# Kernel optimization log

Measured on AMD Instinct MI355X. Metric: run time of the kernel, lower is better.

Reference implementation:

```python
import jax, jax.numpy as jnp
import numpy as np

N_NODES, N_EDGES, NODE_D, EDGE_D, EMB_D, N_GRAPHS = 50000, 800000, 128, 100, 92, 256
N_CONV, FC_D, N_FC, CUTOFF = 3, 128, 2, 6.0


def setup_inputs() -> dict:
    key = jax.random.key(0)
    ks = jax.random.split(key, 24)
    s = 0.05
    inp = {
        "z": jax.random.randint(ks[0], (N_NODES,), 0, 100, dtype=jnp.int32),
        "R": jax.random.normal(ks[1], (N_NODES, 3), dtype=jnp.float32) * 5.0,
        "edge_index": jax.random.randint(ks[2], (2, N_EDGES), 0, N_NODES, dtype=jnp.int32),
        "batch": jnp.sort(jax.random.randint(ks[3], (N_NODES,), 0, N_GRAPHS, dtype=jnp.int32)),
        # learned parameters
        "embedding": jax.random.uniform(ks[4], (100, EMB_D), dtype=jnp.float32),
        "emb_w": jax.random.normal(ks[5], (EMB_D, NODE_D), dtype=jnp.float32) * s,
        "emb_b": jnp.zeros((NODE_D,), jnp.float32),
        "conv_w": jax.random.normal(ks[6], (N_CONV, 2 * NODE_D + EDGE_D, 2 * NODE_D), dtype=jnp.float32) * s,
        "conv_b": jnp.zeros((N_CONV, 2 * NODE_D), jnp.float32),
        "ln_g": jnp.ones((N_CONV, NODE_D), jnp.float32),
        "ln_b": jnp.zeros((N_CONV, NODE_D), jnp.float32),
        "cfc_w": jax.random.normal(ks[7], (NODE_D, FC_D), dtype=jnp.float32) * s,
        "cfc_b": jnp.zeros((FC_D,), jnp.float32),
        "fc_w": jax.random.normal(ks[8], (N_FC, FC_D, FC_D), dtype=jnp.float32) * s,
        "fc_b": jnp.zeros((N_FC, FC_D), jnp.float32),
        "out_w": jax.random.normal(ks[9], (FC_D, 1), dtype=jnp.float32) * s,
        "out_b": jnp.zeros((1,), jnp.float32),
    }
    return inp


def _gaussian_smearing(d):
    offsets = jnp.linspace(0.0, CUTOFF, EDGE_D, dtype=d.dtype)  # [EDGE_D]
    coeff = -0.5 / (offsets[1] - offsets[0]) ** 2
    return jnp.exp(coeff * (d[:, None] - offsets[None, :]) ** 2)  # [E, EDGE_D]


def _layernorm(x, g, b, eps=1e-5):
    mu = x.mean(-1, keepdims=True)
    var = x.var(-1, keepdims=True)
    return (x - mu) / jnp.sqrt(var + eps) * g + b


def reference(z, R, edge_index, batch, embedding, emb_w, emb_b, conv_w, conv_b,
              ln_g, ln_b, cfc_w, cfc_b, fc_w, fc_b, out_w, out_b):
    src, dst = edge_index[0], edge_index[1]  # messages flow src(j) -> dst(i)
    d = jnp.linalg.norm(R[src] - R[dst], axis=-1)  # [E]
    edge_attr = _gaussian_smearing(d)  # [E, EDGE_D]

    x = embedding[z] @ emb_w + emb_b  # [N, NODE_D]
    n = x.shape[0]
    for l in range(conv_w.shape[0]):
        xi, xj = x[dst], x[src]  # gather [E, NODE_D]
        zc = jnp.concatenate([xi, xj, edge_attr], axis=1) @ conv_w[l] + conv_b[l]  # [E, 2*NODE_D]
        z1, z2 = jnp.split(zc, 2, axis=1)
        msg = jax.nn.sigmoid(z1) * jax.nn.softplus(z2)  # [E, NODE_D]
        agg = jax.ops.segment_sum(msg, dst, num_segments=n)  # scatter-add
        x = jax.nn.softplus(_layernorm(agg, ln_g[l], ln_b[l]) + x)

    # global mean pool over graphs
    sums = jax.ops.segment_sum(x, batch, num_segments=N_GRAPHS)
    cnts = jax.ops.segment_sum(jnp.ones((n, 1), x.dtype), batch, num_segments=N_GRAPHS)
    mol = sums / jnp.maximum(cnts, 1.0)  # [N_GRAPHS, NODE_D]

    h = jax.nn.softplus(mol @ cfc_w + cfc_b)
    for l in range(fc_w.shape[0]):
        h = jax.nn.softplus(h @ fc_w[l] + fc_b[l])
    return h @ out_w + out_b  # energy [N_GRAPHS, 1]
```

## Files before the change

### kernel.cpp

```cpp
#include <hip/hip_runtime.h>
#include <hip/hip_bf16.h>
#include <cmath>

#define N_NODES 50000
#define N_EDGES 800000
#define NODE_DIM 128
#define EDGE_DIM 100
#define EMB_DIM 92
#define N_GRAPHS 256

typedef __attribute__((ext_vector_type(8))) short short8_t;
typedef __attribute__((ext_vector_type(4))) float float4_t;

__device__ __forceinline__ float softplus_f(float v) {
    return v > 20.0f ? v : __logf(1.0f + __expf(v));
}
__device__ __forceinline__ float sigmoid_f(float v) {
    return 1.0f / (1.0f + __expf(-v));
}
__device__ __forceinline__ float bflo(unsigned u) { return __uint_as_float(u << 16); }
__device__ __forceinline__ float bfhi(unsigned u) { return __uint_as_float(u & 0xffff0000u); }
__device__ __forceinline__ float hlo(unsigned u) {
    unsigned short s = (unsigned short)(u & 0xffffu);
    _Float16 h; __builtin_memcpy(&h, &s, 2); return (float)h;
}
__device__ __forceinline__ float hhi(unsigned u) {
    unsigned short s = (unsigned short)(u >> 16);
    _Float16 h; __builtin_memcpy(&h, &s, 2); return (float)h;
}

__global__ void deg_kernel(const int* __restrict__ ei, int* __restrict__ deg) {
    int e = blockIdx.x * blockDim.x + threadIdx.x;
    if (e >= N_EDGES) return;
    atomicAdd(&deg[ei[N_EDGES + e]], 1);
}

#define SB 1024
__global__ void scan1_kernel(const int* __restrict__ deg, int* __restrict__ rp,
                             int* __restrict__ bsum) {
    __shared__ int buf[SB];
    int b = blockIdx.x, t = threadIdx.x, i = b * SB + t;
    int v = (i < N_NODES) ? deg[i] : 0;
    buf[t] = v;
    __syncthreads();
    for (int off = 1; off < SB; off <<= 1) {
        int a = (t >= off) ? buf[t - off] : 0;
        __syncthreads();
        buf[t] += a;
        __syncthreads();
    }
    if (i < N_NODES) rp[i] = buf[t] - v;
    if (t == SB - 1) bsum[b] = buf[t];
}
__global__ void scan2_kernel(int* __restrict__ bsum, int n) {
    if (threadIdx.x == 0) {
        int s = 0;
        for (int i = 0; i < n; i++) { int v = bsum[i]; bsum[i] = s; s += v; }
    }
}
__global__ void scan3_kernel(int* __restrict__ rp, const int* __restrict__ bsum) {
    int i = blockIdx.x * SB + threadIdx.x;
    if (i < N_NODES) rp[i] += bsum[blockIdx.x];
    if (i == 0) rp[N_NODES] = N_EDGES;
}

__global__ void fill_kernel(const int* __restrict__ ei, const float* __restrict__ R,
                            const int* __restrict__ row_ptr, int* __restrict__ cnt2,
                            float2* __restrict__ em) {
    int e = blockIdx.x * blockDim.x + threadIdx.x;
    if (e >= N_EDGES) return;
    int s = ei[e];
    int dst = ei[N_EDGES + e];
    float dx = R[3 * s + 0] - R[3 * dst + 0];
    float dy = R[3 * s + 1] - R[3 * dst + 1];
    float dz = R[3 * s + 2] - R[3 * dst + 2];
    float d = sqrtf(dx * dx + dy * dy + dz * dz);
    int pos = row_ptr[dst] + atomicAdd(&cnt2[dst], 1);
    em[pos] = make_float2(__int_as_float(s), d);
}

__global__ void gb_kernel(const int* __restrict__ batch, int* __restrict__ gs) {
    int i = blockIdx.x * 256 + threadIdx.x;
    if (i > N_NODES) return;
    int b = (i < N_NODES) ? batch[i] : N_GRAPHS;
    int pb = (i == 0) ? -1 : batch[i - 1];
    for (int g = pb + 1; g <= b; g++) gs[g] = i;
}

__global__ void wcvt_kernel(const float* __restrict__ conv_w, unsigned* __restrict__ Wep) {
    int i = blockIdx.x * 256 + threadIdx.x;
    if (i >= 3 * EDGE_DIM * 128) return;
    int l = i / (EDGE_DIM * 128), r = i - l * (EDGE_DIM * 128);
    int k = r >> 7, c = r & 127;
    const float* row = conv_w + (size_t)l * 356 * 256 + (size_t)(256 + k) * 256;
    __hip_bfloat16 lo = (__hip_bfloat16)row[c];
    __hip_bfloat16 hi = (__hip_bfloat16)row[128 + c];
    Wep[i] = ((unsigned)*(unsigned short*)&hi << 16) | (unsigned)*(unsigned short*)&lo;
}

__global__ void wprep_kernel(const float* __restrict__ conv_w, short* __restrict__ WbB) {
    int idx = blockIdx.x * 256 + threadIdx.x;
    if (idx >= 3 * 4 * 32 * 64 * 8) return;
    int j = idx & 7;
    int lane = (idx >> 3) & 63;
    int nt = (idx >> 9) & 31;
    int kc = (idx >> 14) & 3;
    int l = idx >> 16;
    int k = kc * 32 + (lane >> 4) * 8 + j;
    int nl = lane & 15;
    int row, col;
    if (nt < 16) { row = k; col = nt * 16 + nl; }
    else { row = 128 + k; col = (nt - 16) * 16 + nl; }
    __hip_bfloat16 bv = (__hip_bfloat16)conv_w[(size_t)l * 356 * 256 + (size_t)row * 256 + col];
    WbB[idx] = *(short*)&bv;
}

__global__ void embed_kernel(const int* __restrict__ z, const float* __restrict__ emb,
                             const float* __restrict__ emb_w, const float* __restrict__ emb_b,
                             float* __restrict__ x, __hip_bfloat16* __restrict__ xb) {
    __shared__ float er[EMB_DIM * 8];
    __shared__ int zi[8];
    int base = blockIdx.x * 8;
    int t = threadIdx.x;
    if (t < 8) zi[t] = z[base + t];
    __syncthreads();
    for (int idx = t; idx < EMB_DIM * 8; idx += 128) {
        int k = idx >> 3, j = idx & 7;
        er[idx] = emb[zi[j] * EMB_DIM + k];
    }
    __syncthreads();
    float acc[8];
    float bb = emb_b[t];
#pragma unroll
    for (int j = 0; j < 8; j++) acc[j] = bb;
    for (int k = 0; k < EMB_DIM; k++) {
        float w = emb_w[k * NODE_DIM + t];
        float4 ja = *(const float4*)&er[k * 8];
        float4 jb = *(const float4*)&er[k * 8 + 4];
        acc[0] = fmaf(w, ja.x, acc[0]); acc[1] = fmaf(w, ja.y, acc[1]);
        acc[2] = fmaf(w, ja.z, acc[2]); acc[3] = fmaf(w, ja.w, acc[3]);
        acc[4] = fmaf(w, jb.x, acc[4]); acc[5] = fmaf(w, jb.y, acc[5]);
        acc[6] = fmaf(w, jb.z, acc[6]); acc[7] = fmaf(w, jb.w, acc[7]);
    }
#pragma unroll
    for (int j = 0; j < 8; j++) {
        x[(base + j) * NODE_DIM + t] = acc[j];
        xb[(base + j) * NODE_DIM + t] = (__hip_bfloat16)acc[j];
    }
}

__global__ __launch_bounds__(256) void node_mfma_kernel(
    const __hip_bfloat16* __restrict__ xb, const short* __restrict__ WbB,
    const float* __restrict__ bl, float* __restrict__ P1f, _Float16* __restrict__ P2h) {
    int t = threadIdx.x;
    int wv = t >> 6, lane = t & 63;
    int mrow = lane & 15, q = lane >> 4;
    int base = blockIdx.x * 16;
    const short* xr = (const short*)xb + (size_t)(base + mrow) * 128 + q * 8;
    float4_t acc[8];
#pragma unroll
    for (int i = 0; i < 8; i++) acc[i] = (float4_t){0.f, 0.f, 0.f, 0.f};
#pragma unroll
    for (int kc = 0; kc < 4; kc++) {
        short8_t a = *(const short8_t*)(xr + kc * 32);
#pragma unroll
        for (int i = 0; i < 8; i++) {
            int nt = wv * 8 + i;
            short8_t b = *(const short8_t*)&WbB[((size_t)(kc * 32 + nt) * 64 + lane) * 8];
            acc[i] = __builtin_amdgcn_mfma_f32_16x16x32_bf16(a, b, acc[i], 0, 0, 0);
        }
    }
#pragma unroll
    for (int i = 0; i < 8; i++) {
        int nt = wv * 8 + i;
        int np = nt * 16 + mrow;
        if (np < 256) {
            float bb = bl[np];
            int off = 2 * (np & 127) + (np >> 7);
#pragma unroll
            for (int r = 0; r < 4; r++)
                P1f[(size_t)(base + q * 4 + r) * 256 + off] = acc[i][r] + bb;
        } else {
            int np2 = np - 256;
            int off = 2 * (np2 & 127) + (np2 >> 7);
#pragma unroll
            for (int r = 0; r < 4; r++)
                P2h[(size_t)(base + q * 4 + r) * 256 + off] = (_Float16)acc[i][r];
        }
    }
}

#define NTAP 10
__device__ __forceinline__ void edge_msg2(uint2 bu, float dv, float4 a,
                                          const uint2* __restrict__ Wc,
                                          float& acc0, float& acc1) {
    const float sp_ = 6.0f / 99.0f;
    const float inv_s = 99.0f / 6.0f;
    const float coeff = -0.5f * inv_s * inv_s;
    float z10 = a.x + hlo(bu.x), z20 = a.y + hhi(bu.x);
    float z11 = a.z + hlo(bu.y), z21 = a.w + hhi(bu.y);
    if (dv <= 6.34f) {
        int k0 = max(0, min(EDGE_DIM - NTAP, (int)ceilf(dv * inv_s - 4.5f)));
        const uint2* wr = Wc + k0 * 64;
#pragma unroll
        for (int i = 0; i < NTAP; i++) {
            float df = dv - (float)(k0 + i) * sp_;
            float ee = __expf(coeff * df * df);
            uint2 u = wr[i * 64];
            z10 = fmaf(bflo(u.x), ee, z10);
            z20 = fmaf(bfhi(u.x), ee, z20);
            z11 = fmaf(bflo(u.y), ee, z11);
            z21 = fmaf(bfhi(u.y), ee, z21);
        }
    }
    acc0 += sigmoid_f(z10) * softplus_f(z20);
    acc1 += sigmoid_f(z11) * softplus_f(z21);
}

__global__ __launch_bounds__(256) void node_edge_ln_kernel(
    const int* __restrict__ row_ptr, const float2* __restrict__ em,
    const float4* __restrict__ P1q, const uint2* __restrict__ P2q,
    const uint2* __restrict__ Weq,
    const float* __restrict__ lg, const float* __restrict__ lb,
    float* __restrict__ x, __hip_bfloat16* __restrict__ xb) {
    int node = blockIdx.x * 4 + (threadIdx.x >> 6);
    int l = threadIdx.x & 63;
    int c0 = 2 * l;
    int e0 = row_ptr[node], e1 = row_ptr[node + 1];
    float4 a = P1q[(size_t)node * 64 + l];
    const uint2* Wc = Weq + l;
    float acc0 = 0.f, acc1 = 0.f;
    uint2 bA = make_uint2(0, 0), bB = make_uint2(0, 0);
    float dvA = 0.f, dvB = 0.f;
    int srcC = 0, srcD = 0;
    float dC = 0.f, dD = 0.f;
    if (e0 < e1) {
        float2 m = em[e0];
        int s = __float_as_int(m.x); dvA = m.y;
        bA = P2q[(size_t)s * 64 + l];
    }
    if (e0 + 1 < e1) {
        float2 m = em[e0 + 1];
        int s = __float_as_int(m.x); dvB = m.y;
        bB = P2q[(size_t)s * 64 + l];
    }
    if (e0 + 2 < e1) { float2 m = em[e0 + 2]; srcC = __float_as_int(m.x); dC = m.y; }
    if (e0 + 3 < e1) { float2 m = em[e0 + 3]; srcD = __float_as_int(m.x); dD = m.y; }
    int e = e0;
    while (e < e1) {
        {
            uint2 b = bA; float dv = dvA;
            if (e + 2 < e1) { bA = P2q[(size_t)srcC * 64 + l]; dvA = dC; }
            if (e + 4 < e1) { float2 m = em[e + 4]; srcC = __float_as_int(m.x); dC = m.y; }
            edge_msg2(b, dv, a, Wc, acc0, acc1);
        }
        e++;
        if (e >= e1) break;
        {
            uint2 b = bB; float dv = dvB;
            if (e + 2 < e1) { bB = P2q[(size_t)srcD * 64 + l]; dvB = dD; }
            if (e + 4 < e1) { float2 m = em[e + 4]; srcD = __float_as_int(m.x); dD = m.y; }
            edge_msg2(b, dv, a, Wc, acc0, acc1);
        }
        e++;
    }
    float s1 = acc0 + acc1;
    float s2 = acc0 * acc0 + acc1 * acc1;
#pragma unroll
    for (int off = 32; off > 0; off >>= 1) {
        s1 += __shfl_xor(s1, off);
        s2 += __shfl_xor(s2, off);
    }
    float mu = s1 * (1.0f / 128.0f);
    float var = s2 * (1.0f / 128.0f) - mu * mu;
    float rstd = rsqrtf(fmaxf(var, 0.f) + 1e-5f);
    float2 xv = *(const float2*)&x[(size_t)node * 128 + c0];
    float2 gg = *(const float2*)&lg[c0];
    float2 bb = *(const float2*)&lb[c0];
    float r0 = softplus_f((acc0 - mu) * rstd * gg.x + bb.x + xv.x);
    float r1 = softplus_f((acc1 - mu) * rstd * gg.y + bb.y + xv.y);
    *(float2*)&x[(size_t)node * 128 + c0] = make_float2(r0, r1);
    __hip_bfloat16 h0 = (__hip_bfloat16)r0, h1 = (__hip_bfloat16)r1;
    unsigned pk = ((unsigned)*(unsigned short*)&h1 << 16) | (unsigned)*(unsigned short*)&h0;
    *(unsigned*)&xb[(size_t)node * 128 + c0] = pk;
}

__global__ void pool_head_kernel(const float* __restrict__ x, const int* __restrict__ gs,
                                 const float* __restrict__ cfc_w, const float* __restrict__ cfc_b,
                                 const float* __restrict__ fc_w, const float* __restrict__ fc_b,
                                 const float* __restrict__ out_w, const float* __restrict__ out_b,
                                 float* __restrict__ out) {
    int g = blockIdx.x, c = threadIdx.x;
    int n0 = gs[g], n1 = gs[g + 1];
    float s = 0.f;
    for (int n = n0; n < n1; n++) s += x[(size_t)n * 128 + c];
    __shared__ float h[128], h2[128];
    h[c] = s / fmaxf((float)(n1 - n0), 1.0f);
    __syncthreads();
    float acc = cfc_b[c];
    for (int k = 0; k < 128; k++) acc = fmaf(h[k], cfc_w[k * 128 + c], acc);
    h2[c] = softplus_f(acc);
    __syncthreads();
    for (int l = 0; l < 2; l++) {
        const float* W = fc_w + l * 128 * 128;
        acc = fc_b[l * 128 + c];
        for (int k = 0; k < 128; k++) acc = fmaf(h2[k], W[k * 128 + c], acc);
        __syncthreads();
        h2[c] = softplus_f(acc);
        __syncthreads();
    }
    h[c] = h2[c] * out_w[c];
    __syncthreads();
    for (int off = 64; off > 0; off >>= 1) {
        if (c < off) h[c] += h[c + off];
        __syncthreads();
    }
    if (c == 0) out[g] = h[0] + out_b[0];
}

extern "C" void kernel_launch(void* const* d_in, const int* in_sizes, int n_in,
                              void* d_out, int out_size, void* d_ws, size_t ws_size,
                              hipStream_t stream) {
    const int*   z      = (const int*)d_in[0];
    const float* R      = (const float*)d_in[1];
    const int*   ei     = (const int*)d_in[2];
    const int*   batch  = (const int*)d_in[3];
    const float* emb    = (const float*)d_in[4];
    const float* emb_w  = (const float*)d_in[5];
    const float* emb_b  = (const float*)d_in[6];
    const float* conv_w = (const float*)d_in[7];
    const float* conv_b = (const float*)d_in[8];
    const float* ln_g   = (const float*)d_in[9];
    const float* ln_b   = (const float*)d_in[10];
    const float* cfc_w  = (const float*)d_in[11];
    const float* cfc_b  = (const float*)d_in[12];
    const float* fc_w   = (const float*)d_in[13];
    const float* fc_b   = (const float*)d_in[14];
    const float* out_w  = (const float*)d_in[15];
    const float* out_b  = (const float*)d_in[16];
    float* out = (float*)d_out;

    float* ws    = (float*)d_ws;
    float* x     = ws;
    float* agg   = x + 6400000;
    float* P1f   = agg + 6400000;
    _Float16* P2h = (_Float16*)(P1f + 12800000);
    float* emf   = (float*)(P2h + 12800000);
    int* s_dst   = (int*)(emf + 1600000);
    int* row_ptr = s_dst + 800000;
    int* deg     = row_ptr + 50004;
    int* cnt2    = deg + 50000;
    int* bsum    = cnt2 + 50000;
    int* gs      = bsum + 64;
    unsigned* Wep        = (unsigned*)(gs + 260);
    short* WbB           = (short*)(Wep + 38400);
    __hip_bfloat16* xb   = (__hip_bfloat16*)(WbB + 196608);
    float2* em = (float2*)emf;

    hipMemsetAsync(deg, 0, (size_t)100000 * 4, stream);
    deg_kernel<<<(N_EDGES + 255) / 256, 256, 0, stream>>>(ei, deg);
    int nsb = (N_NODES + SB - 1) / SB;
    scan1_kernel<<<nsb, SB, 0, stream>>>(deg, row_ptr, bsum);
    scan2_kernel<<<1, 64, 0, stream>>>(bsum, nsb);
    scan3_kernel<<<nsb, SB, 0, stream>>>(row_ptr, bsum);
    fill_kernel<<<(N_EDGES + 255) / 256, 256, 0, stream>>>(ei, R, row_ptr, cnt2, em);
    gb_kernel<<<(N_NODES + 256) / 256 + 1, 256, 0, stream>>>(batch, gs);
    wcvt_kernel<<<(3 * EDGE_DIM * 128 + 255) / 256, 256, 0, stream>>>(conv_w, Wep);
    wprep_kernel<<<(3 * 4 * 32 * 64 * 8 + 255) / 256, 256, 0, stream>>>(conv_w, WbB);

    embed_kernel<<<N_NODES / 8, 128, 0, stream>>>(z, emb, emb_w, emb_b, x, xb);
    for (int l = 0; l < 3; l++) {
        node_mfma_kernel<<<N_NODES / 16, 256, 0, stream>>>(xb, WbB + (size_t)l * 65536,
                                                           conv_b + l * 256, P1f, P2h);
        node_edge_ln_kernel<<<N_NODES / 4, 256, 0, stream>>>(
            row_ptr, em, (const float4*)P1f, (const uint2*)P2h,
            (const uint2*)(Wep + (size_t)l * EDGE_DIM * 128),
            ln_g + l * 128, ln_b + l * 128, x, xb);
    }
    pool_head_kernel<<<N_GRAPHS, 128, 0, stream>>>(x, gs, cfc_w, cfc_b, fc_w, fc_b,
                                                   out_w, out_b, out);
}
```

Measured before the change: 966.1 us.

## Process four edges concurrently per wavefront with 8 channels per lane

The per-node edge-aggregation kernel is restructured so each wavefront splits into four 16-lane groups. Each group handles a different edge, and each lane covers 8 channels using 128-bit loads of P2 and the weights. Partial sums are then reduced across groups with shuffles before the layernorm. The aim is more memory-level parallelism per wave and fewer serial iterations for high-degree nodes, at the cost of higher register pressure. Padded tail edges are computed and then masked out, which wastes some work on nodes whose degree is not a multiple of four.

```diff
diff --git a/kernel.cpp b/kernel.cpp
--- a/kernel.cpp
+++ b/kernel.cpp
@@ -191,98 +191,140 @@
 }
 
 #define NTAP 10
-__device__ __forceinline__ void edge_msg2(uint2 bu, float dv, float4 a,
-                                          const uint2* __restrict__ Wc,
-                                          float& acc0, float& acc1) {
+__global__ __launch_bounds__(256) void node_edge_ln_kernel(
+    const int* __restrict__ row_ptr, const float2* __restrict__ em,
+    const float4* __restrict__ P1v, const uint4* __restrict__ P2v,
+    const uint4* __restrict__ Wev,
+    const float* __restrict__ lg, const float* __restrict__ lb,
+    float* __restrict__ x, __hip_bfloat16* __restrict__ xb) {
     const float sp_ = 6.0f / 99.0f;
     const float inv_s = 99.0f / 6.0f;
     const float coeff = -0.5f * inv_s * inv_s;
-    float z10 = a.x + hlo(bu.x), z20 = a.y + hhi(bu.x);
-    float z11 = a.z + hlo(bu.y), z21 = a.w + hhi(bu.y);
-    if (dv <= 6.34f) {
-        int k0 = max(0, min(EDGE_DIM - NTAP, (int)ceilf(dv * inv_s - 4.5f)));
-        const uint2* wr = Wc + k0 * 64;
-#pragma unroll
-        for (int i = 0; i < NTAP; i++) {
-            float df = dv - (float)(k0 + i) * sp_;
-            float ee = __expf(coeff * df * df);
-            uint2 u = wr[i * 64];
-            z10 = fmaf(bflo(u.x), ee, z10);
-            z20 = fmaf(bfhi(u.x), ee, z20);
-            z11 = fmaf(bflo(u.y), ee, z11);
-            z21 = fmaf(bfhi(u.y), ee, z21);
-        }
-    }
-    acc0 += sigmoid_f(z10) * softplus_f(z20);
-    acc1 += sigmoid_f(z11) * softplus_f(z21);
-}
-
-__global__ __launch_bounds__(256) void node_edge_ln_kernel(
-    const int* __restrict__ row_ptr, const float2* __restrict__ em,
-    const float4* __restrict__ P1q, const uint2* __restrict__ P2q,
-    const uint2* __restrict__ Weq,
-    const float* __restrict__ lg, const float* __restrict__ lb,
-    float* __restrict__ x, __hip_bfloat16* __restrict__ xb) {
     int node = blockIdx.x * 4 + (threadIdx.x >> 6);
     int l = threadIdx.x & 63;
-    int c0 = 2 * l;
+    int g = l >> 4, i = l & 15;
     int e0 = row_ptr[node], e1 = row_ptr[node + 1];
-    float4 a = P1q[(size_t)node * 64 + l];
-    const uint2* Wc = Weq + l;
-    float acc0 = 0.f, acc1 = 0.f;
-    uint2 bA = make_uint2(0, 0), bB = make_uint2(0, 0);
-    float dvA = 0.f, dvB = 0.f;
-    int srcC = 0, srcD = 0;
-    float dC = 0.f, dD = 0.f;
+    float4 A0 = P1v[(size_t)node * 64 + 2 * i];
+    float4 A1 = P1v[(size_t)node * 64 + 2 * i + 1];
+    float4 A2 = P1v[(size_t)node * 64 + 32 + 2 * i];
+    float4 A3 = P1v[(size_t)node * 64 + 33 + 2 * i];
+    float4 accP = make_float4(0.f, 0.f, 0.f, 0.f);
+    float4 accQ = make_float4(0.f, 0.f, 0.f, 0.f);
+
     if (e0 < e1) {
-        float2 m = em[e0];
-        int s = __float_as_int(m.x); dvA = m.y;
-        bA = P2q[(size_t)s * 64 + l];
-    }
-    if (e0 + 1 < e1) {
-        float2 m = em[e0 + 1];
-        int s = __float_as_int(m.x); dvB = m.y;
-        bB = P2q[(size_t)s * 64 + l];
-    }
-    if (e0 + 2 < e1) { float2 m = em[e0 + 2]; srcC = __float_as_int(m.x); dC = m.y; }
-    if (e0 + 3 < e1) { float2 m = em[e0 + 3]; srcD = __float_as_int(m.x); dD = m.y; }
-    int e = e0;
-    while (e < e1) {
-        {
-            uint2 b = bA; float dv = dvA;
-            if (e + 2 < e1) { bA = P2q[(size_t)srcC * 64 + l]; dvA = dC; }
-            if (e + 4 < e1) { float2 m = em[e + 4]; srcC = __float_as_int(m.x); dC = m.y; }
-            edge_msg2(b, dv, a, Wc, acc0, acc1);
+        int emax = e1 - 1;
+        int srcA, srcB; float dvAm, dvBm;
+        uint4 dA0, dA1, dB0, dB1; float dvAd, dvBd;
+        { float2 m = em[min(e0 + g, emax)];      srcA = __float_as_int(m.x); dvAm = m.y; }
+        { float2 m = em[min(e0 + 4 + g, emax)];  srcB = __float_as_int(m.x); dvBm = m.y; }
+        dA0 = P2v[(size_t)srcA * 32 + i]; dA1 = P2v[(size_t)srcA * 32 + 16 + i]; dvAd = dvAm;
+        { float2 m = em[min(e0 + 8 + g, emax)];  srcA = __float_as_int(m.x); dvAm = m.y; }
+        dB0 = P2v[(size_t)srcB * 32 + i]; dB1 = P2v[(size_t)srcB * 32 + 16 + i]; dvBd = dvBm;
+        { float2 m = em[min(e0 + 12 + g, emax)]; srcB = __float_as_int(m.x); dvBm = m.y; }
+
+#define PHASE(S, eb_)                                                             \
+        {                                                                         \
+            uint4 d0 = d##S##0, d1 = d##S##1; float dvv = dv##S##d;               \
+            d##S##0 = P2v[(size_t)src##S * 32 + i];                               \
+            d##S##1 = P2v[(size_t)src##S * 32 + 16 + i];                          \
+            dv##S##d = dv##S##m;                                                  \
+            { float2 m = em[min((eb_) + 16 + g, emax)];                           \
+              src##S = __float_as_int(m.x); dv##S##m = m.y; }                     \
+            float vm = ((eb_) + g < e1) ? 1.0f : 0.0f;                            \
+            float z10 = A0.x + hlo(d0.x), z20 = A0.y + hhi(d0.x);                 \
+            float z11 = A0.z + hlo(d0.y), z21 = A0.w + hhi(d0.y);                 \
+            float z12 = A1.x + hlo(d0.z), z22 = A1.y + hhi(d0.z);                 \
+            float z13 = A1.z + hlo(d0.w), z23 = A1.w + hhi(d0.w);                 \
+            float z14 = A2.x + hlo(d1.x), z24 = A2.y + hhi(d1.x);                 \
+            float z15 = A2.z + hlo(d1.y), z25 = A2.w + hhi(d1.y);                 \
+            float z16 = A3.x + hlo(d1.z), z26 = A3.y + hhi(d1.z);                 \
+            float z17 = A3.z + hlo(d1.w), z27 = A3.w + hhi(d1.w);                 \
+            if (dvv <= 6.34f) {                                                   \
+                int k0 = max(0, min(EDGE_DIM - NTAP, (int)ceilf(dvv * inv_s - 4.5f))); \
+                const uint4* wr = Wev + k0 * 32 + i;                              \
+                _Pragma("unroll")                                                 \
+                for (int t_ = 0; t_ < NTAP; t_++) {                               \
+                    uint4 w0 = wr[t_ * 32]; uint4 w1 = wr[t_ * 32 + 16];          \
+                    float df = dvv - (float)(k0 + t_) * sp_;                      \
+                    float ee = __expf(coeff * df * df);                           \
+                    z10 = fmaf(bflo(w0.x), ee, z10); z20 = fmaf(bfhi(w0.x), ee, z20); \
+                    z11 = fmaf(bflo(w0.y), ee, z11); z21 = fmaf(bfhi(w0.y), ee, z21); \
+                    z12 = fmaf(bflo(w0.z), ee, z12); z22 = fmaf(bfhi(w0.z), ee, z22); \
+                    z13 = fmaf(bflo(w0.w), ee, z13); z23 = fmaf(bfhi(w0.w), ee, z23); \
+                    z14 = fmaf(bflo(w1.x), ee, z14); z24 = fmaf(bfhi(w1.x), ee, z24); \
+                    z15 = fmaf(bflo(w1.y), ee, z15); z25 = fmaf(bfhi(w1.y), ee, z25); \
+                    z16 = fmaf(bflo(w1.z), ee, z16); z26 = fmaf(bfhi(w1.z), ee, z26); \
+                    z17 = fmaf(bflo(w1.w), ee, z17); z27 = fmaf(bfhi(w1.w), ee, z27); \
+                }                                                                 \
+            }                                                                     \
+            accP.x += vm * sigmoid_f(z10) * softplus_f(z20);                      \
+            accP.y += vm * sigmoid_f(z11) * softplus_f(z21);                      \
+            accP.z += vm * sigmoid_f(z12) * softplus_f(z22);                      \
+            accP.w += vm * sigmoid_f(z13) * softplus_f(z23);                      \
+            accQ.x += vm * sigmoid_f(z14) * softplus_f(z24);                      \
+            accQ.y += vm * sigmoid_f(z15) * softplus_f(z25);                      \
+            accQ.z += vm * sigmoid_f(z16) * softplus_f(z26);                      \
+            accQ.w += vm * sigmoid_f(z17) * softplus_f(z27);                      \
         }
-        e++;
-        if (e >= e1) break;
-        {
-            uint2 b = bB; float dv = dvB;
-            if (e + 2 < e1) { bB = P2q[(size_t)srcD * 64 + l]; dvB = dD; }
-            if (e + 4 < e1) { float2 m = em[e + 4]; srcD = __float_as_int(m.x); dD = m.y; }
-            edge_msg2(b, dv, a, Wc, acc0, acc1);
+
+        int eb = e0;
+        while (true) {
+            PHASE(A, eb);
+            eb += 4; if (eb >= e1) break;
+            PHASE(B, eb);
+            eb += 4; if (eb >= e1) break;
         }
-        e++;
-    }
-    float s1 = acc0 + acc1;
-    float s2 = acc0 * acc0 + acc1 * acc1;
-#pragma unroll
-    for (int off = 32; off > 0; off >>= 1) {
+#undef PHASE
+    }
+
+    accP.x += __shfl_xor(accP.x, 16); accP.x += __shfl_xor(accP.x, 32);
+    accP.y += __shfl_xor(accP.y, 16); accP.y += __shfl_xor(accP.y, 32);
+    accP.z += __shfl_xor(accP.z, 16); accP.z += __shfl_xor(accP.z, 32);
+    accP.w += __shfl_xor(accP.w, 16); accP.w += __shfl_xor(accP.w, 32);
+    accQ.x += __shfl_xor(accQ.x, 16); accQ.x += __shfl_xor(accQ.x, 32);
+    accQ.y += __shfl_xor(accQ.y, 16); accQ.y += __shfl_xor(accQ.y, 32);
+    accQ.z += __shfl_xor(accQ.z, 16); accQ.z += __shfl_xor(accQ.z, 32);
+    accQ.w += __shfl_xor(accQ.w, 16); accQ.w += __shfl_xor(accQ.w, 32);
+    float s1 = accP.x + accP.y + accP.z + accP.w + accQ.x + accQ.y + accQ.z + accQ.w;
+    float s2 = accP.x * accP.x + accP.y * accP.y + accP.z * accP.z + accP.w * accP.w +
+               accQ.x * accQ.x + accQ.y * accQ.y + accQ.z * accQ.z + accQ.w * accQ.w;
+#pragma unroll
+    for (int off = 8; off > 0; off >>= 1) {
         s1 += __shfl_xor(s1, off);
         s2 += __shfl_xor(s2, off);
     }
     float mu = s1 * (1.0f / 128.0f);
     float var = s2 * (1.0f / 128.0f) - mu * mu;
     float rstd = rsqrtf(fmaxf(var, 0.f) + 1e-5f);
-    float2 xv = *(const float2*)&x[(size_t)node * 128 + c0];
-    float2 gg = *(const float2*)&lg[c0];
-    float2 bb = *(const float2*)&lb[c0];
-    float r0 = softplus_f((acc0 - mu) * rstd * gg.x + bb.x + xv.x);
-    float r1 = softplus_f((acc1 - mu) * rstd * gg.y + bb.y + xv.y);
-    *(float2*)&x[(size_t)node * 128 + c0] = make_float2(r0, r1);
-    __hip_bfloat16 h0 = (__hip_bfloat16)r0, h1 = (__hip_bfloat16)r1;
-    unsigned pk = ((unsigned)*(unsigned short*)&h1 << 16) | (unsigned)*(unsigned short*)&h0;
-    *(unsigned*)&xb[(size_t)node * 128 + c0] = pk;
+    float4 xv1 = *(const float4*)&x[(size_t)node * 128 + 4 * i];
+    float4 xv2 = *(const float4*)&x[(size_t)node * 128 + 64 + 4 * i];
+    float4 g1 = *(const float4*)&lg[4 * i];
+    float4 g2 = *(const float4*)&lg[64 + 4 * i];
+    float4 b1 = *(const float4*)&lb[4 * i];
+    float4 b2 = *(const float4*)&lb[64 + 4 * i];
+    float r0 = softplus_f((accP.x - mu) * rstd * g1.x + b1.x + xv1.x);
+    float r1 = softplus_f((accP.y - mu) * rstd * g1.y + b1.y + xv1.y);
+    float r2 = softplus_f((accP.z - mu) * rstd * g1.z + b1.z + xv1.z);
+    float r3 = softplus_f((accP.w - mu) * rstd * g1.w + b1.w + xv1.w);
+    float r4 = softplus_f((accQ.x - mu) * rstd * g2.x + b2.x + xv2.x);
+    float r5 = softplus_f((accQ.y - mu) * rstd * g2.y + b2.y + xv2.y);
+    float r6 = softplus_f((accQ.z - mu) * rstd * g2.z + b2.z + xv2.z);
+    float r7 = softplus_f((accQ.w - mu) * rstd * g2.w + b2.w + xv2.w);
+    if (g == 0) {
+        *(float4*)&x[(size_t)node * 128 + 4 * i] = make_float4(r0, r1, r2, r3);
+        *(float4*)&x[(size_t)node * 128 + 64 + 4 * i] = make_float4(r4, r5, r6, r7);
+        __hip_bfloat16 h0 = (__hip_bfloat16)r0, h1 = (__hip_bfloat16)r1;
+        __hip_bfloat16 h2 = (__hip_bfloat16)r2, h3 = (__hip_bfloat16)r3;
+        __hip_bfloat16 h4 = (__hip_bfloat16)r4, h5 = (__hip_bfloat16)r5;
+        __hip_bfloat16 h6 = (__hip_bfloat16)r6, h7 = (__hip_bfloat16)r7;
+        uint2 pk1, pk2;
+        pk1.x = ((unsigned)*(unsigned short*)&h1 << 16) | (unsigned)*(unsigned short*)&h0;
+        pk1.y = ((unsigned)*(unsigned short*)&h3 << 16) | (unsigned)*(unsigned short*)&h2;
+        pk2.x = ((unsigned)*(unsigned short*)&h5 << 16) | (unsigned)*(unsigned short*)&h4;
+        pk2.y = ((unsigned)*(unsigned short*)&h7 << 16) | (unsigned)*(unsigned short*)&h6;
+        *(uint2*)&xb[(size_t)node * 128 + 4 * i] = pk1;
+        *(uint2*)&xb[(size_t)node * 128 + 64 + 4 * i] = pk2;
+    }
 }
 
 __global__ void pool_head_kernel(const float* __restrict__ x, const int* __restrict__ gs,
@@ -373,8 +415,8 @@
         node_mfma_kernel<<<N_NODES / 16, 256, 0, stream>>>(xb, WbB + (size_t)l * 65536,
                                                            conv_b + l * 256, P1f, P2h);
         node_edge_ln_kernel<<<N_NODES / 4, 256, 0, stream>>>(
-            row_ptr, em, (const float4*)P1f, (const uint2*)P2h,
-            (const uint2*)(Wep + (size_t)l * EDGE_DIM * 128),
+            row_ptr, em, (const float4*)P1f, (const uint4*)P2h,
+            (const uint4*)(Wep + (size_t)l * EDGE_DIM * 128),
             ln_g + l * 128, ln_b + l * 128, x, xb);
     }
     pool_head_kernel<<<N_GRAPHS, 128, 0, stream>>>(x, gs, cfc_w, cfc_b, fc_w, fc_b,
```

Result: slower. 1.009 ms (+4.4%).

## Stage edge weights in LDS and deepen gather prefetch pipeline in edge kernel

Applied to the files above, without the earlier changes.

The edge-aggregation kernel now copies the per-layer bf16 edge weight slice (about 51 KB) into shared memory and reads the taps from LDS instead of global memory. The per-edge metadata and source-row gathers are software-pipelined in batches of 8 edges with two ping-pong register sets and scheduling barriers. Edge indices and row bounds are scalarized with readfirstlane so the gather addresses use scalar registers. The large LDS footprint and register count may lower occupancy, and each 4-node block repeats the weight copy.

```diff
diff --git a/kernel.cpp b/kernel.cpp
--- a/kernel.cpp
+++ b/kernel.cpp
@@ -191,79 +191,129 @@
 }
 
 #define NTAP 10
-__device__ __forceinline__ void edge_msg2(uint2 bu, float dv, float4 a,
-                                          const uint2* __restrict__ Wc,
-                                          float& acc0, float& acc1) {
+__global__ __launch_bounds__(256) void node_edge_ln_kernel(
+    const int* __restrict__ row_ptr, const float2* __restrict__ em,
+    const float4* __restrict__ P1v, const uint2* __restrict__ P2q,
+    const unsigned* __restrict__ Wep,
+    const float* __restrict__ lg, const float* __restrict__ lb,
+    float* __restrict__ x, __hip_bfloat16* __restrict__ xb) {
+    __shared__ unsigned WeL[EDGE_DIM * 128];
+    {
+        const uint4* s4 = (const uint4*)Wep;
+        uint4* d4 = (uint4*)WeL;
+        for (int i = threadIdx.x; i < EDGE_DIM * 32; i += 256) d4[i] = s4[i];
+    }
+    __syncthreads();
+    const uint2* WeL2 = (const uint2*)WeL;
     const float sp_ = 6.0f / 99.0f;
     const float inv_s = 99.0f / 6.0f;
     const float coeff = -0.5f * inv_s * inv_s;
-    float z10 = a.x + hlo(bu.x), z20 = a.y + hhi(bu.x);
-    float z11 = a.z + hlo(bu.y), z21 = a.w + hhi(bu.y);
-    if (dv <= 6.34f) {
-        int k0 = max(0, min(EDGE_DIM - NTAP, (int)ceilf(dv * inv_s - 4.5f)));
-        const uint2* wr = Wc + k0 * 64;
-#pragma unroll
-        for (int i = 0; i < NTAP; i++) {
-            float df = dv - (float)(k0 + i) * sp_;
-            float ee = __expf(coeff * df * df);
-            uint2 u = wr[i * 64];
-            z10 = fmaf(bflo(u.x), ee, z10);
-            z20 = fmaf(bfhi(u.x), ee, z20);
-            z11 = fmaf(bflo(u.y), ee, z11);
-            z21 = fmaf(bfhi(u.y), ee, z21);
-        }
-    }
-    acc0 += sigmoid_f(z10) * softplus_f(z20);
-    acc1 += sigmoid_f(z11) * softplus_f(z21);
-}
-
-__global__ __launch_bounds__(256) void node_edge_ln_kernel(
-    const int* __restrict__ row_ptr, const float2* __restrict__ em,
-    const float4* __restrict__ P1q, const uint2* __restrict__ P2q,
-    const uint2* __restrict__ Weq,
-    const float* __restrict__ lg, const float* __restrict__ lb,
-    float* __restrict__ x, __hip_bfloat16* __restrict__ xb) {
     int node = blockIdx.x * 4 + (threadIdx.x >> 6);
     int l = threadIdx.x & 63;
-    int c0 = 2 * l;
-    int e0 = row_ptr[node], e1 = row_ptr[node + 1];
-    float4 a = P1q[(size_t)node * 64 + l];
-    const uint2* Wc = Weq + l;
+    int e0 = __builtin_amdgcn_readfirstlane(row_ptr[node]);
+    int e1 = __builtin_amdgcn_readfirstlane(row_ptr[node + 1]);
+    float4 a = P1v[(size_t)node * 64 + l];
+    float2 xv = *(const float2*)&x[(size_t)node * 128 + 2 * l];
+    float2 gg = *(const float2*)&lg[2 * l];
+    float2 bv = *(const float2*)&lb[2 * l];
     float acc0 = 0.f, acc1 = 0.f;
-    uint2 bA = make_uint2(0, 0), bB = make_uint2(0, 0);
-    float dvA = 0.f, dvB = 0.f;
-    int srcC = 0, srcD = 0;
-    float dC = 0.f, dD = 0.f;
+
     if (e0 < e1) {
-        float2 m = em[e0];
-        int s = __float_as_int(m.x); dvA = m.y;
-        bA = P2q[(size_t)s * 64 + l];
-    }
-    if (e0 + 1 < e1) {
-        float2 m = em[e0 + 1];
-        int s = __float_as_int(m.x); dvB = m.y;
-        bB = P2q[(size_t)s * 64 + l];
-    }
-    if (e0 + 2 < e1) { float2 m = em[e0 + 2]; srcC = __float_as_int(m.x); dC = m.y; }
-    if (e0 + 3 < e1) { float2 m = em[e0 + 3]; srcD = __float_as_int(m.x); dD = m.y; }
-    int e = e0;
-    while (e < e1) {
-        {
-            uint2 b = bA; float dv = dvA;
-            if (e + 2 < e1) { bA = P2q[(size_t)srcC * 64 + l]; dvA = dC; }
-            if (e + 4 < e1) { float2 m = em[e + 4]; srcC = __float_as_int(m.x); dC = m.y; }
-            edge_msg2(b, dv, a, Wc, acc0, acc1);
+        const int emax = e1 - 1;
+        float2 mA0, mA1, mA2, mA3, mA4, mA5, mA6, mA7;
+        float2 mB0, mB1, mB2, mB3, mB4, mB5, mB6, mB7;
+        int sA0, sA1, sA2, sA3, sA4, sA5, sA6, sA7;
+        int sB0, sB1, sB2, sB3, sB4, sB5, sB6, sB7;
+        float dA0, dA1, dA2, dA3, dA4, dA5, dA6, dA7;
+        float dB0, dB1, dB2, dB3, dB4, dB5, dB6, dB7;
+        uint2 rA0, rA1, rA2, rA3, rA4, rA5, rA6, rA7;
+        uint2 rB0, rB1, rB2, rB3, rB4, rB5, rB6, rB7;
+
+#define MISSUE(X, base_)                                                      \
+        m##X##0 = em[min((base_) + 0, emax)];                                 \
+        m##X##1 = em[min((base_) + 1, emax)];                                 \
+        m##X##2 = em[min((base_) + 2, emax)];                                 \
+        m##X##3 = em[min((base_) + 3, emax)];                                 \
+        m##X##4 = em[min((base_) + 4, emax)];                                 \
+        m##X##5 = em[min((base_) + 5, emax)];                                 \
+        m##X##6 = em[min((base_) + 6, emax)];                                 \
+        m##X##7 = em[min((base_) + 7, emax)];
+
+#define SCAL1(X, j)                                                           \
+        s##X##j = __builtin_amdgcn_readfirstlane(__float_as_int(m##X##j.x));  \
+        d##X##j = __int_as_float(__builtin_amdgcn_readfirstlane(__float_as_int(m##X##j.y)));
+
+#define SCALARIZE(X)                                                          \
+        SCAL1(X, 0) SCAL1(X, 1) SCAL1(X, 2) SCAL1(X, 3)                       \
+        SCAL1(X, 4) SCAL1(X, 5) SCAL1(X, 6) SCAL1(X, 7)
+
+#define RISSUE(X)                                                             \
+        r##X##0 = P2q[(size_t)s##X##0 * 64 + l];                              \
+        r##X##1 = P2q[(size_t)s##X##1 * 64 + l];                              \
+        r##X##2 = P2q[(size_t)s##X##2 * 64 + l];                              \
+        r##X##3 = P2q[(size_t)s##X##3 * 64 + l];                              \
+        r##X##4 = P2q[(size_t)s##X##4 * 64 + l];                              \
+        r##X##5 = P2q[(size_t)s##X##5 * 64 + l];                              \
+        r##X##6 = P2q[(size_t)s##X##6 * 64 + l];                              \
+        r##X##7 = P2q[(size_t)s##X##7 * 64 + l];
+
+#define EMSG(rr, dd, idx_)                                                    \
+        if ((idx_) < e1) {                                                    \
+            float z10 = a.x + hlo((rr).x), z20 = a.y + hhi((rr).x);           \
+            float z11 = a.z + hlo((rr).y), z21 = a.w + hhi((rr).y);           \
+            if ((dd) <= 6.34f) {                                              \
+                int k0 = max(0, min(EDGE_DIM - NTAP, (int)ceilf((dd) * inv_s - 4.5f))); \
+                const uint2* wr = WeL2 + k0 * 64 + l;                         \
+                _Pragma("unroll")                                             \
+                for (int t_ = 0; t_ < NTAP; t_++) {                           \
+                    uint2 u = wr[t_ * 64];                                    \
+                    float df = (dd) - (float)(k0 + t_) * sp_;                 \
+                    float ee = __expf(coeff * df * df);                       \
+                    z10 = fmaf(bflo(u.x), ee, z10); z20 = fmaf(bfhi(u.x), ee, z20); \
+                    z11 = fmaf(bflo(u.y), ee, z11); z21 = fmaf(bfhi(u.y), ee, z21); \
+                }                                                             \
+            }                                                                 \
+            acc0 += sigmoid_f(z10) * softplus_f(z20);                         \
+            acc1 += sigmoid_f(z11) * softplus_f(z21);                         \
         }
-        e++;
-        if (e >= e1) break;
-        {
-            uint2 b = bB; float dv = dvB;
-            if (e + 2 < e1) { bB = P2q[(size_t)srcD * 64 + l]; dvB = dD; }
-            if (e + 4 < e1) { float2 m = em[e + 4]; srcD = __float_as_int(m.x); dD = m.y; }
-            edge_msg2(b, dv, a, Wc, acc0, acc1);
+
+#define COMPUTE(X, eb_)                                                       \
+        EMSG(r##X##0, d##X##0, (eb_) + 0) EMSG(r##X##1, d##X##1, (eb_) + 1)   \
+        EMSG(r##X##2, d##X##2, (eb_) + 2) EMSG(r##X##3, d##X##3, (eb_) + 3)   \
+        EMSG(r##X##4, d##X##4, (eb_) + 4) EMSG(r##X##5, d##X##5, (eb_) + 5)   \
+        EMSG(r##X##6, d##X##6, (eb_) + 6) EMSG(r##X##7, d##X##7, (eb_) + 7)
+
+        MISSUE(A, e0)
+        MISSUE(B, e0 + 8)
+        __builtin_amdgcn_sched_barrier(0);
+        SCALARIZE(A)
+        RISSUE(A)
+        __builtin_amdgcn_sched_barrier(0);
+        int eb = e0;
+        while (true) {
+            MISSUE(A, eb + 16)
+            __builtin_amdgcn_sched_barrier(0);
+            SCALARIZE(B)
+            RISSUE(B)
+            __builtin_amdgcn_sched_barrier(0);
+            COMPUTE(A, eb)
+            eb += 8; if (eb >= e1) break;
+            MISSUE(B, eb + 16)
+            __builtin_amdgcn_sched_barrier(0);
+            SCALARIZE(A)
+            RISSUE(A)
+            __builtin_amdgcn_sched_barrier(0);
+            COMPUTE(B, eb)
+            eb += 8; if (eb >= e1) break;
         }
-        e++;
-    }
+#undef MISSUE
+#undef SCAL1
+#undef SCALARIZE
+#undef RISSUE
+#undef EMSG
+#undef COMPUTE
+    }
+
     float s1 = acc0 + acc1;
     float s2 = acc0 * acc0 + acc1 * acc1;
 #pragma unroll
@@ -274,15 +324,12 @@
     float mu = s1 * (1.0f / 128.0f);
     float var = s2 * (1.0f / 128.0f) - mu * mu;
     float rstd = rsqrtf(fmaxf(var, 0.f) + 1e-5f);
-    float2 xv = *(const float2*)&x[(size_t)node * 128 + c0];
-    float2 gg = *(const float2*)&lg[c0];
-    float2 bb = *(const float2*)&lb[c0];
-    float r0 = softplus_f((acc0 - mu) * rstd * gg.x + bb.x + xv.x);
-    float r1 = softplus_f((acc1 - mu) * rstd * gg.y + bb.y + xv.y);
-    *(float2*)&x[(size_t)node * 128 + c0] = make_float2(r0, r1);
+    float r0 = softplus_f((acc0 - mu) * rstd * gg.x + bv.x + xv.x);
+    float r1 = softplus_f((acc1 - mu) * rstd * gg.y + bv.y + xv.y);
+    *(float2*)&x[(size_t)node * 128 + 2 * l] = make_float2(r0, r1);
     __hip_bfloat16 h0 = (__hip_bfloat16)r0, h1 = (__hip_bfloat16)r1;
     unsigned pk = ((unsigned)*(unsigned short*)&h1 << 16) | (unsigned)*(unsigned short*)&h0;
-    *(unsigned*)&xb[(size_t)node * 128 + c0] = pk;
+    *(unsigned*)&xb[(size_t)node * 128 + 2 * l] = pk;
 }
 
 __global__ void pool_head_kernel(const float* __restrict__ x, const int* __restrict__ gs,
@@ -374,7 +421,7 @@
                                                            conv_b + l * 256, P1f, P2h);
         node_edge_ln_kernel<<<N_NODES / 4, 256, 0, stream>>>(
             row_ptr, em, (const float4*)P1f, (const uint2*)P2h,
-            (const uint2*)(Wep + (size_t)l * EDGE_DIM * 128),
+            Wep + (size_t)l * EDGE_DIM * 128,
             ln_g + l * 128, ln_b + l * 128, x, xb);
     }
     pool_head_kernel<<<N_GRAPHS, 128, 0, stream>>>(x, gs, cfc_w, cfc_b, fc_w, fc_b,
```

Measured after the change: 929.4 us. 3.8% less time.
